# Optimization experiments

Measured on AMD Instinct MI355X. Metric: run time of the kernel, lower is better.

Reference implementation:

```python
import jax, jax.numpy as jnp
import numpy as np

B, S, D, H, F, E, K = 2, 2048, 1024, 16, 4096, 8, 2
EPS = 1e-6


def setup_inputs() -> dict:
    key = jax.random.key(0)
    ks = jax.random.split(key, 9)
    s = 0.02
    return {
        "x": jax.random.normal(ks[0], (B, S, D), jnp.float32),
        "n1_w": jnp.ones((D,), jnp.float32),
        "n2_w": jnp.ones((D,), jnp.float32),
        "wq": jax.random.normal(ks[1], (D, D), jnp.float32) * s,
        "wk": jax.random.normal(ks[2], (D, D), jnp.float32) * s,
        "wv": jax.random.normal(ks[3], (D, D), jnp.float32) * s,
        "wo": jax.random.normal(ks[4], (D, D), jnp.float32) * s,
        "router_w": jax.random.normal(ks[5], (E, D), jnp.float32) * s,  # nn.Linear(D, E, bias=False)
        "w1": jax.random.normal(ks[6], (E, D, F), jnp.float32) * s,
        "b1": jnp.zeros((E, F), jnp.float32),
        "w2": jax.random.normal(ks[7], (E, F, D), jnp.float32) * s,
        "b2": jnp.zeros((E, D), jnp.float32),
    }


def _rms(t, w):
    return t * w * jax.lax.rsqrt(jnp.mean(t * t, axis=-1, keepdims=True) + EPS)


def reference(x, n1_w, n2_w, wq, wk, wv, wo, router_w, w1, b1, w2, b2):
    hd = D // H
    # --- pre-norm causal multi-head self-attention ---
    h = _rms(x, n1_w)
    q = (h @ wq).reshape(B, S, H, hd)
    k = (h @ wk).reshape(B, S, H, hd)
    v = (h @ wv).reshape(B, S, H, hd)
    scores = jnp.einsum("bqhd,bkhd->bhqk", q, k) * (hd ** -0.5)
    causal = jnp.tril(jnp.ones((S, S), bool))
    scores = jnp.where(causal, scores, jnp.float32(-1e9))
    attn = jax.nn.softmax(scores, axis=-1)
    attn_out = jnp.einsum("bhqk,bkhd->bqhd", attn, v).reshape(B, S, D) @ wo
    x = x + attn_out
    # --- pre-norm MoE MLP: dense experts + top-k weighted combine ---
    h2 = _rms(x, n2_w)
    logits = h2 @ router_w.T                         # [B,S,E]
    probs = jax.nn.softmax(logits, axis=-1)
    topv, topi = jax.lax.top_k(probs, K)             # [B,S,K]
    topv = topv / jnp.sum(topv, axis=-1, keepdims=True)  # renormalized top-k gates
    bi = jnp.arange(B)[:, None, None]
    si = jnp.arange(S)[None, :, None]
    gates = jnp.zeros_like(probs).at[bi, si, topi].set(topv)  # sparse gates [B,S,E]
    eh = jax.nn.gelu(jnp.einsum("bsd,edf->ebsf", h2, w1) + b1[:, None, None, :])
    eo = jnp.einsum("ebsf,efd->ebsd", eh, w2) + b2[:, None, None, :]
    y = jnp.einsum("ebsd,bse->bsd", eo, gates)
    return x + y
```

## Files before the change

### kernel.cpp

```cpp
#include <hip/hip_runtime.h>
#include <hip/hip_bf16.h>


typedef float fx4 __attribute__((ext_vector_type(4)));
typedef short sx4 __attribute__((ext_vector_type(4)));
typedef short sx8 __attribute__((ext_vector_type(8)));
typedef int ix2 __attribute__((ext_vector_type(2)));
typedef int ix4 __attribute__((ext_vector_type(4)));

#define DEVFN static __device__ __forceinline__
#define MFMA16(a, b, c) __builtin_amdgcn_mfma_f32_16x16x32_bf16((a), (b), (c), 0, 0, 0)

typedef __attribute__((address_space(1))) const void GASV;
typedef __attribute__((address_space(3))) void LASV;

DEVFN short f2bf(float f) {
  unsigned u = __float_as_uint(f);
  return (short)((u + 0x7FFFu + ((u >> 16) & 1u)) >> 16);
}
DEVFN float bf2f(short s) { return __uint_as_float(((unsigned)(unsigned short)s) << 16); }

DEVFN int cvt_pk_bf16(float a, float b) {
  int r;
  asm("v_cvt_pk_bf16_f32 %0, %1, %2" : "=v"(r) : "v"(a), "v"(b));
  return r;
}

DEVFN void gll16(const short* g, short* l) {
  __builtin_amdgcn_global_load_lds((GASV*)g, (LASV*)l, 16, 0, 0);
}

DEVFN float fast_gelu(float x) {
  float u = 0.7978845608028654f * (x + 0.044715f * x * x * x);
  float e = __expf(2.0f * u);
  float t = 1.0f - 2.0f / (1.0f + e);
  return 0.5f * x * (1.0f + t);
}

DEVFN float wsum64(float v) {
#pragma unroll
  for (int m = 1; m < 64; m <<= 1) v += __shfl_xor(v, m);
  return v;
}

template <int SPLIT>
__global__ __launch_bounds__(256) void transpose_k(const float* in, short* oh, short* ol,
                                                   int R, int C) {
  __shared__ float t[64][65];
  const int c0 = blockIdx.x * 64, r0 = blockIdx.y * 64;
  const long long bofs = (long long)blockIdx.z * R * C;
  in += bofs;
  oh += bofs;
  if (SPLIT) ol += bofs;
  const int tid = threadIdx.x;
  const int rr = tid >> 4, cc4 = (tid & 15) * 4;
#pragma unroll
  for (int i = 0; i < 4; ++i) {
    int r = i * 16 + rr;
    fx4 v = *(const fx4*)(in + (long long)(r0 + r) * C + c0 + cc4);
    t[r][cc4] = v.x;
    t[r][cc4 + 1] = v.y;
    t[r][cc4 + 2] = v.z;
    t[r][cc4 + 3] = v.w;
  }
  __syncthreads();
#pragma unroll
  for (int i = 0; i < 4; ++i) {
    int oc = i * 16 + rr;
    sx4 hv, lv;
#pragma unroll
    for (int j = 0; j < 4; ++j) {
      float v = t[cc4 + j][oc];
      short hi = f2bf(v);
      hv[j] = hi;
      if (SPLIT) lv[j] = f2bf(v - bf2f(hi));
    }
    *(sx4*)(oh + (long long)(c0 + oc) * R + r0 + cc4) = hv;
    if (SPLIT) *(sx4*)(ol + (long long)(c0 + oc) * R + r0 + cc4) = lv;
  }
}

template <int SPLIT>
__global__ __launch_bounds__(256) void rms_k(const float* x, const float* w, short* hh,
                                             short* hl) {
  const int row = blockIdx.x, tid = threadIdx.x;
  const fx4 v = ((const fx4*)(x + (long long)row * 1024))[tid];
  float ss = v.x * v.x + v.y * v.y + v.z * v.z + v.w * v.w;
  ss = wsum64(ss);
  __shared__ float red[4];
  if ((tid & 63) == 0) red[tid >> 6] = ss;
  __syncthreads();
  ss = red[0] + red[1] + red[2] + red[3];
  const float rr = rsqrtf(ss * (1.0f / 1024.0f) + 1e-6f);
  const fx4 wv = ((const fx4*)w)[tid];
  float vals[4] = {v.x * wv.x * rr, v.y * wv.y * rr, v.z * wv.z * rr, v.w * wv.w * rr};
  sx4 oh, ol;
#pragma unroll
  for (int c = 0; c < 4; ++c) {
    short hi = f2bf(vals[c]);
    oh[c] = hi;
    if (SPLIT) ol[c] = f2bf(vals[c] - bf2f(hi));
  }
  ((sx4*)(hh + (long long)row * 1024))[tid] = oh;
  if (SPLIT) ((sx4*)(hl + (long long)row * 1024))[tid] = ol;
}

struct GemmArgs {
  const short *Ah, *Al, *Bh, *Bl;
  int K, lda, ldb, ldc;
  long long strideBe;
  short *out_h, *out_l;
  float* out_f;
  const float* bias;
  const int* tile_info;
  const float* row_gate;
};

template <int TERMS, int BK, int BN, int EPI, int PIPE>
__global__ __launch_bounds__(256) void gemm_k(GemmArgs a) {
  const int tid = threadIdx.x, lane = tid & 63, wave = tid >> 6;
  const int gx = gridDim.x;
  const int nwg = gx * (int)gridDim.y;
  int flat = (int)blockIdx.y * gx + (int)blockIdx.x;
  flat = (flat & 7) * (nwg >> 3) + (flat >> 3);
  const int bx = flat % gx;
  const int by = flat / gx;

  int row0, expert = 0, valid = 128;
  if constexpr (EPI == 3 || EPI == 5) {
    const int* ti = a.tile_info + by * 4;
    expert = ti[0];
    row0 = ti[1];
    valid = ti[2];
    if (valid == 0) return;
  } else {
    row0 = by * 128;
  }
  const short* Ap = a.Ah;
  const short* Bp = a.Bh + ((EPI == 3 || EPI == 5) ? (long long)expert * a.strideBe : 0ll);
  const int kbeg = blockIdx.z * a.K;

  constexpr int CH = BK / 8;
  constexpr int SW = (BK == 64) ? 7 : 3;
  constexpr int NIA = BK / 16;
  constexpr int NIB = (BN * CH) / 256;
  constexpr int ASZ = 128 * BK;
  constexpr int BSZ = BN * BK;
  constexpr int TN = BN / 32;
  constexpr int NB = PIPE ? 2 : 1;

  __shared__ short Ash[NB][ASZ];
  __shared__ short Bsh[NB][BSZ];
  __shared__ short Asl[TERMS == 3 ? NB : 1][TERMS == 3 ? ASZ : 1];
  __shared__ short Bsl[TERMS == 3 ? NB : 1][TERMS == 3 ? BSZ : 1];

  fx4 acc[4][TN] = {};
  const int wr = wave >> 1, wc = wave & 1;

  auto stage = [&](int s, int k0) {
#pragma unroll
    for (int i = 0; i < NIA; ++i) {
      int t = i * 256 + tid;
      int row = t / CH, c = t % CH;
      int cc = c ^ (row & SW);
      int lbase = (i * 256 + wave * 64) * 8;
      long long acol = kbeg + k0 + cc * 8;
      gll16(Ap + (long long)(row0 + row) * a.lda + acol, &Ash[s][lbase]);
      if constexpr (TERMS == 3)
        gll16(a.Al + (long long)(row0 + row) * a.lda + acol, &Asl[s][lbase]);
    }
#pragma unroll
    for (int i = 0; i < NIB; ++i) {
      int t = i * 256 + tid;
      int row = t / CH, c = t % CH;
      int cc = c ^ (row & SW);
      int lbase = (i * 256 + wave * 64) * 8;
      long long acol = kbeg + k0 + cc * 8;
      gll16(Bp + (long long)(bx * BN + row) * a.ldb + acol, &Bsh[s][lbase]);
      if constexpr (TERMS == 3)
        gll16(a.Bl + (long long)(bx * BN + row) * a.ldb + acol, &Bsl[s][lbase]);
    }
  };

  auto compute = [&](int s) {
#pragma unroll
    for (int kk = 0; kk < BK / 32; ++kk) {
      sx8 ah[4], bh[TN], al_[4], bl_[TN];
#pragma unroll
      for (int mi = 0; mi < 4; ++mi) {
        int row = wr * 64 + mi * 16 + (lane & 15);
        int sc = (kk * 4 + (lane >> 4)) ^ (row & SW);
        ah[mi] = *(const sx8*)&Ash[s][row * BK + sc * 8];
        if constexpr (TERMS == 3) al_[mi] = *(const sx8*)&Asl[s][row * BK + sc * 8];
      }
#pragma unroll
      for (int ni = 0; ni < TN; ++ni) {
        int row = wc * (BN / 2) + ni * 16 + (lane & 15);
        int sc = (kk * 4 + (lane >> 4)) ^ (row & SW);
        bh[ni] = *(const sx8*)&Bsh[s][row * BK + sc * 8];
        if constexpr (TERMS == 3) bl_[ni] = *(const sx8*)&Bsl[s][row * BK + sc * 8];
      }
#pragma unroll
      for (int mi = 0; mi < 4; ++mi)
#pragma unroll
        for (int ni = 0; ni < TN; ++ni) {
          acc[mi][ni] = MFMA16(ah[mi], bh[ni], acc[mi][ni]);
          if constexpr (TERMS == 3) {
            acc[mi][ni] = MFMA16(ah[mi], bl_[ni], acc[mi][ni]);
            acc[mi][ni] = MFMA16(al_[mi], bh[ni], acc[mi][ni]);
          }
        }
    }
  };

  const int NT = a.K / BK;
  stage(0, 0);
  __syncthreads();
  for (int t = 0; t < NT; ++t) {
    if constexpr (PIPE) {
      if (t + 1 < NT) stage((t + 1) & 1, (t + 1) * BK);
      compute(t & 1);
      if (t + 1 < NT) __syncthreads();
    } else {
      compute(0);
      if (t + 1 < NT) {
        __syncthreads();
        stage(0, (t + 1) * BK);
        __syncthreads();
      }
    }
  }

#pragma unroll
  for (int mi = 0; mi < 4; ++mi)
#pragma unroll
    for (int ni = 0; ni < TN; ++ni) {
      fx4 v = acc[mi][ni];
      int rl = wr * 64 + mi * 16 + ((lane >> 4) << 2);
      int col = bx * BN + wc * (BN / 2) + ni * 16 + (lane & 15);
#pragma unroll
      for (int j = 0; j < 4; ++j) {
        int r = rl + j;
        long long grow = (long long)row0 + r;
        float xv = v[j];
        if constexpr (EPI == 1) {
          short hi = f2bf(xv);
          a.out_h[grow * a.ldc + col] = hi;
          a.out_l[grow * a.ldc + col] = f2bf(xv - bf2f(hi));
        } else if constexpr (EPI == 3) {
          xv += a.bias[expert * a.ldc + col];
          a.out_h[grow * a.ldc + col] = f2bf(fast_gelu(xv));
        } else if constexpr (EPI == 5) {
          if (r < valid) {
            xv += a.bias[expert * a.ldc + col];
            float g = a.row_gate[grow];
            a.out_h[grow * a.ldc + col] = f2bf(xv * g);
          }
        } else if constexpr (EPI == 6) {
          a.out_f[(long long)blockIdx.z * 4194304 + grow * a.ldc + col] = xv;
        }
      }
    }
}

__global__ __launch_bounds__(256) void combine_wo_k(const float* p0, const float* p1,
                                                    const float* resid, float* out) {
  const long long i = ((long long)blockIdx.x * 256 + threadIdx.x) * 4;
  fx4 a = *(const fx4*)(p0 + i);
  fx4 b = *(const fx4*)(p1 + i);
  fx4 r = *(const fx4*)(resid + i);
  fx4 o;
#pragma unroll
  for (int j = 0; j < 4; ++j) o[j] = a[j] + b[j] + r[j];
  *(fx4*)(out + i) = o;
}

__global__ __launch_bounds__(256) void combine_k(const int* row_of_entry,
                                                 const short* eo, float* out) {
  const int tid = threadIdx.x, lane = tid & 63, wave = tid >> 6;
  const long long token = (long long)blockIdx.x * 4 + wave;
  const int r1 = row_of_entry[token * 2];
  const int r2 = row_of_entry[token * 2 + 1];
  const sx8* e1 = (const sx8*)(eo + (long long)r1 * 1024);
  const sx8* e2 = (const sx8*)(eo + (long long)r2 * 1024);
  float* op = out + token * 1024;
#pragma unroll
  for (int half = 0; half < 2; ++half) {
    sx8 va = e1[lane + half * 64];
    sx8 vb = e2[lane + half * 64];
    int cb = (lane + half * 64) * 8;
#pragma unroll
    for (int q = 0; q < 2; ++q) {
      fx4 o = *(const fx4*)(op + cb + q * 4);
#pragma unroll
      for (int j = 0; j < 4; ++j) o[j] += bf2f(va[q * 4 + j]) + bf2f(vb[q * 4 + j]);
      *(fx4*)(op + cb + q * 4) = o;
    }
  }
}

__global__ __launch_bounds__(128, 2) void flash_k(const short* __restrict__ qkv_h,
                                                  const short* __restrict__ qkv_l,
                                                  short* __restrict__ ao_h,
                                                  short* __restrict__ ao_l) {
  const int tid = threadIdx.x, lane = tid & 63, wave = tid >> 6;
  const int l15 = lane & 15, g = lane >> 4;
  const int qt = (blockIdx.x + blockIdx.y) & 31;
  const int bh = blockIdx.y;
  const int b = bh >> 4, h = bh & 15;
  const long long base = (long long)b * 2048 * 3072;
  const int qw = qt * 64 + wave * 32;

  __shared__ short Kh[4096], Kl[4096];
  __shared__ int VTh[64 * 34], VTl[64 * 34];

  sx8 qh[2][2], ql[2][2];
#pragma unroll
  for (int mb = 0; mb < 2; ++mb)
#pragma unroll
    for (int kk = 0; kk < 2; ++kk) {
      long long qofs =
          base + (long long)(qw + mb * 16 + l15) * 3072 + h * 64 + kk * 32 + g * 8;
      qh[mb][kk] = *(const sx8*)(qkv_h + qofs);
      ql[mb][kk] = *(const sx8*)(qkv_l + qofs);
    }

  fx4 o[2][4] = {};
  float m_r[2] = {-3e38f, -3e38f}, l_r[2] = {0.f, 0.f};

  const int krow0 = tid >> 3;
  const int kc8 = (tid & 7) * 8;
  const int kswz = ((tid & 7) ^ (krow0 & 7)) * 8;
  const int vu = tid >> 3;
  const int vd0 = (tid & 7) * 8;

  sx8 kr[4], krl[4], vr[4], vrl[4];

  auto load_tile = [&](int kt2) {
    const long long tb = base + (long long)(kt2 * 64) * 3072 + h * 64;
#pragma unroll
    for (int s = 0; s < 4; ++s) {
      long long gofs = tb + 1024 + (long long)(s * 16 + krow0) * 3072 + kc8;
      kr[s] = *(const sx8*)(qkv_h + gofs);
      krl[s] = *(const sx8*)(qkv_l + gofs);
    }
#pragma unroll
    for (int k4 = 0; k4 < 4; ++k4) {
      long long gofs = tb + 2048 + (long long)(4 * vu + k4) * 3072 + vd0;
      vr[k4] = *(const sx8*)(qkv_h + gofs);
      vrl[k4] = *(const sx8*)(qkv_l + gofs);
    }
  };

  const int nt = qt + 1;
  load_tile(0);

  for (int kt = 0; kt < nt; ++kt) {
#pragma unroll
    for (int s = 0; s < 4; ++s) {
      *(sx8*)&Kh[(s * 16 + krow0) * 64 + kswz] = kr[s];
      *(sx8*)&Kl[(s * 16 + krow0) * 64 + kswz] = krl[s];
    }
#pragma unroll
    for (int i = 0; i < 8; ++i) {
      int d = vd0 + i;
      ix2 wh, wl;
      wh[0] = (int)(unsigned short)vr[0][i] | ((int)(unsigned short)vr[1][i] << 16);
      wh[1] = (int)(unsigned short)vr[2][i] | ((int)(unsigned short)vr[3][i] << 16);
      wl[0] = (int)(unsigned short)vrl[0][i] | ((int)(unsigned short)vrl[1][i] << 16);
      wl[1] = (int)(unsigned short)vrl[2][i] | ((int)(unsigned short)vrl[3][i] << 16);
      *(ix2*)&VTh[d * 34 + 2 * vu] = wh;
      *(ix2*)&VTl[d * 34 + 2 * vu] = wl;
    }
    __syncthreads();

    if (kt + 1 < nt) load_tile(kt + 1);

    const bool diag = (kt == nt - 1);
    float pvv[2][16];
#pragma unroll
    for (int kc = 0; kc < 4; ++kc) {
      int row = kc * 16 + l15;
      int rsw = row & 7;
      fx4 s0 = {}, s1 = {};
#pragma unroll
      for (int kk = 0; kk < 2; ++kk) {
        int sc = ((kk * 4 + g) ^ rsw) * 8;
        sx8 khf = *(const sx8*)&Kh[row * 64 + sc];
        sx8 klf = *(const sx8*)&Kl[row * 64 + sc];
        s0 = MFMA16(khf, qh[0][kk], s0);
        s1 = MFMA16(khf, qh[1][kk], s1);
        s0 = MFMA16(khf, ql[0][kk], s0);
        s1 = MFMA16(khf, ql[1][kk], s1);
        s0 = MFMA16(klf, qh[0][kk], s0);
        s1 = MFMA16(klf, qh[1][kk], s1);
      }
#pragma unroll
      for (int j = 0; j < 4; ++j) {
        pvv[0][kc * 4 + j] = s0[j];
        pvv[1][kc * 4 + j] = s1[j];
      }
    }

    sx8 pah[2][2], pal[2][2];
#pragma unroll
    for (int mb = 0; mb < 2; ++mb) {
      const int qidx = qw + mb * 16 + l15;
      float t[16];
      float tmax = -3e38f;
#pragma unroll
      for (int i = 0; i < 16; ++i) {
        float sv = pvv[mb][i] * 0.18033688011112f;
        if (diag) {
          int key = kt * 64 + (i >> 2) * 16 + g * 4 + (i & 3);
          sv = (key > qidx) ? -3e38f : sv;
        }
        t[i] = sv;
        tmax = fmaxf(tmax, sv);
      }
      tmax = fmaxf(tmax, __shfl_xor(tmax, 16));
      tmax = fmaxf(tmax, __shfl_xor(tmax, 32));
      if (__any(tmax > m_r[mb] + 8.0f)) {
        float mnew = fmaxf(m_r[mb], tmax);
        float al = exp2f(m_r[mb] - mnew);
        l_r[mb] *= al;
        float aj[4];
#pragma unroll
        for (int j = 0; j < 4; ++j) aj[j] = __shfl(al, (lane & 48) | (g << 2) | j);
#pragma unroll
        for (int f = 0; f < 4; ++f)
#pragma unroll
          for (int j = 0; j < 4; ++j) o[mb][f][j] *= aj[j];
        m_r[mb] = mnew;
      }
      float ps = 0.f;
#pragma unroll
      for (int i = 0; i < 16; ++i) {
        float e = exp2f(t[i] - m_r[mb]);
        t[i] = e;
        ps += e;
      }
      l_r[mb] += ps;
#pragma unroll
      for (int grp = 0; grp < 2; ++grp) {
        ix4 ih, il;
#pragma unroll
        for (int q2 = 0; q2 < 4; ++q2) {
          float a = t[grp * 8 + 2 * q2], bb = t[grp * 8 + 2 * q2 + 1];
          int I = cvt_pk_bf16(a, bb);
          float h0 = __uint_as_float((unsigned)I << 16);
          float h1 = __uint_as_float((unsigned)I & 0xffff0000u);
          int L = cvt_pk_bf16(a - h0, bb - h1);
          ih[q2] = I;
          il[q2] = L;
        }
        pah[mb][grp] = __builtin_bit_cast(sx8, ih);
        pal[mb][grp] = __builtin_bit_cast(sx8, il);
      }
    }

    const ix2* vth = (const ix2*)VTh;
    const ix2* vtl = (const ix2*)VTl;
#pragma unroll
    for (int f = 0; f < 4; ++f) {
      int dd = f * 16 + l15;
      ix2 a0 = vth[dd * 17 + g], a1 = vth[dd * 17 + 4 + g];
      ix2 a2 = vth[dd * 17 + 8 + g], a3 = vth[dd * 17 + 12 + g];
      ix2 c0 = vtl[dd * 17 + g], c1 = vtl[dd * 17 + 4 + g];
      ix2 c2 = vtl[dd * 17 + 8 + g], c3 = vtl[dd * 17 + 12 + g];
      ix4 w;
      w[0] = a0[0]; w[1] = a0[1]; w[2] = a1[0]; w[3] = a1[1];
      sx8 vh8a = __builtin_bit_cast(sx8, w);
      w[0] = a2[0]; w[1] = a2[1]; w[2] = a3[0]; w[3] = a3[1];
      sx8 vh8b = __builtin_bit_cast(sx8, w);
      w[0] = c0[0]; w[1] = c0[1]; w[2] = c1[0]; w[3] = c1[1];
      sx8 vl8a = __builtin_bit_cast(sx8, w);
      w[0] = c2[0]; w[1] = c2[1]; w[2] = c3[0]; w[3] = c3[1];
      sx8 vl8b = __builtin_bit_cast(sx8, w);
#pragma unroll
      for (int mb = 0; mb < 2; ++mb) {
        o[mb][f] = MFMA16(pah[mb][0], vh8a, o[mb][f]);
        o[mb][f] = MFMA16(pah[mb][0], vl8a, o[mb][f]);
        o[mb][f] = MFMA16(pal[mb][0], vh8a, o[mb][f]);
        o[mb][f] = MFMA16(pah[mb][1], vh8b, o[mb][f]);
        o[mb][f] = MFMA16(pah[mb][1], vl8b, o[mb][f]);
        o[mb][f] = MFMA16(pal[mb][1], vh8b, o[mb][f]);
      }
    }
    __syncthreads();
  }

#pragma unroll
  for (int mb = 0; mb < 2; ++mb) {
    float lt = l_r[mb];
    lt += __shfl_xor(lt, 16);
    lt += __shfl_xor(lt, 32);
    float linv = 1.0f / lt;
    float lj[4];
#pragma unroll
    for (int j = 0; j < 4; ++j) lj[j] = __shfl(linv, (lane & 48) | (g << 2) | j);
#pragma unroll
    for (int f = 0; f < 4; ++f)
#pragma unroll
      for (int j = 0; j < 4; ++j) {
        float val = o[mb][f][j] * lj[j];
        long long orow = (long long)b * 2048 + qw + mb * 16 + g * 4 + j;
        int ocol = h * 64 + f * 16 + l15;
        short hi = f2bf(val);
        ao_h[orow * 1024 + ocol] = hi;
        ao_l[orow * 1024 + ocol] = f2bf(val - bf2f(hi));
      }
  }
}

__global__ __launch_bounds__(256) void router_k(const float* x2, const float* w,
                                                const float* rw, int* tok_e,
                                                float* tok_g) {
  const int tid = threadIdx.x, lane = tid & 63, wave = tid >> 6;
  const long long token = (long long)blockIdx.x * 4 + wave;
  const fx4* xr = (const fx4*)(x2 + token * 1024);
  const fx4* wr4 = (const fx4*)w;
  fx4 t[4];
  float ss = 0.0f;
#pragma unroll
  for (int i = 0; i < 4; ++i) {
    fx4 xv = xr[i * 64 + lane];
    fx4 wv = wr4[i * 64 + lane];
    ss += xv.x * xv.x + xv.y * xv.y + xv.z * xv.z + xv.w * xv.w;
    t[i].x = xv.x * wv.x;
    t[i].y = xv.y * wv.y;
    t[i].z = xv.z * wv.z;
    t[i].w = xv.w * wv.w;
  }
  ss = wsum64(ss);
  const float rr = rsqrtf(ss * (1.0f / 1024.0f) + 1e-6f);
  float logit[8];
#pragma unroll
  for (int e = 0; e < 8; ++e) {
    const fx4* re = (const fx4*)(rw + e * 1024);
    float acc = 0.0f;
#pragma unroll
    for (int i = 0; i < 4; ++i) {
      fx4 rv = re[i * 64 + lane];
      acc += t[i].x * rv.x + t[i].y * rv.y + t[i].z * rv.z + t[i].w * rv.w;
    }
    logit[e] = wsum64(acc) * rr;
  }
  float mx = logit[0];
#pragma unroll
  for (int e = 1; e < 8; ++e) mx = fmaxf(mx, logit[e]);
  float pe[8];
#pragma unroll
  for (int e = 0; e < 8; ++e) pe[e] = expf(logit[e] - mx);
  int e1 = 0;
  float b1v = pe[0];
#pragma unroll
  for (int e = 1; e < 8; ++e)
    if (pe[e] > b1v) {
      b1v = pe[e];
      e1 = e;
    }
  int e2 = -1;
  float b2v = -1.0f;
#pragma unroll
  for (int e = 0; e < 8; ++e)
    if (e != e1 && pe[e] > b2v) {
      b2v = pe[e];
      e2 = e;
    }
  if (lane == 0) {
    float inv = 1.0f / (b1v + b2v);
    tok_e[token * 2] = e1;
    tok_e[token * 2 + 1] = e2;
    tok_g[token * 2] = b1v * inv;
    tok_g[token * 2 + 1] = b2v * inv;
  }
}

__global__ __launch_bounds__(1024) void rank_k(const int* tok_e, const float* tok_g,
                                               int* tinfo, int* row_of_entry,
                                               int* row_token, float* row_gate) {
  const int tid = threadIdx.x, lane = tid & 63, wave = tid >> 6;
  __shared__ unsigned wtot[16][4];
  __shared__ unsigned woff[16][4];
  __shared__ int segsh[8];
  int e[8];
  {
    const int4* te = (const int4*)tok_e;
    int4 a = te[tid * 2], b = te[tid * 2 + 1];
    e[0] = a.x; e[1] = a.y; e[2] = a.z; e[3] = a.w;
    e[4] = b.x; e[5] = b.y; e[6] = b.z; e[7] = b.w;
  }
  unsigned c0 = 0, c1 = 0, c2 = 0, c3 = 0;
#pragma unroll
  for (int i = 0; i < 8; ++i) {
    unsigned f = 1u << ((e[i] & 1) << 4);
    int h = e[i] >> 1;
    c0 += (h == 0) ? f : 0u;
    c1 += (h == 1) ? f : 0u;
    c2 += (h == 2) ? f : 0u;
    c3 += (h == 3) ? f : 0u;
  }
  unsigned s0 = c0, s1 = c1, s2 = c2, s3 = c3;
#pragma unroll
  for (int d = 1; d < 64; d <<= 1) {
    unsigned t0 = __shfl_up(s0, d), t1 = __shfl_up(s1, d);
    unsigned t2 = __shfl_up(s2, d), t3 = __shfl_up(s3, d);
    if (lane >= d) { s0 += t0; s1 += t1; s2 += t2; s3 += t3; }
  }
  if (lane == 63) {
    wtot[wave][0] = s0; wtot[wave][1] = s1; wtot[wave][2] = s2; wtot[wave][3] = s3;
  }
  __syncthreads();
  if (wave == 0 && lane < 16) {
    unsigned v0 = wtot[lane][0], v1 = wtot[lane][1];
    unsigned v2 = wtot[lane][2], v3 = wtot[lane][3];
    unsigned i0 = v0, i1 = v1, i2 = v2, i3 = v3;
#pragma unroll
    for (int d = 1; d < 16; d <<= 1) {
      unsigned t0 = __shfl_up(i0, d), t1 = __shfl_up(i1, d);
      unsigned t2 = __shfl_up(i2, d), t3 = __shfl_up(i3, d);
      if (lane >= d) { i0 += t0; i1 += t1; i2 += t2; i3 += t3; }
    }
    woff[lane][0] = i0 - v0; woff[lane][1] = i1 - v1;
    woff[lane][2] = i2 - v2; woff[lane][3] = i3 - v3;
    if (lane == 15) {
      wtot[0][0] = i0; wtot[0][1] = i1; wtot[0][2] = i2; wtot[0][3] = i3;
    }
  }
  __syncthreads();
  if (tid == 0) {
    int cnt[8], tte[8], total = 0;
    for (int ee = 0; ee < 8; ++ee) {
      unsigned tot = wtot[0][ee >> 1];
      cnt[ee] = (int)((tot >> ((ee & 1) * 16)) & 0xFFFFu);
      tte[ee] = (cnt[ee] + 127) >> 7;
      total += tte[ee];
    }
    for (int s2 = 0; s2 < 80; ++s2) tinfo[s2 * 4 + 2] = 0;
    int off = 0, i = 0;
    for (int ee = 0; ee < 8; ++ee) {
      segsh[ee] = off;
      for (int t2 = 0; t2 < tte[ee]; ++t2) {
        int slot = (i * 80) / total;
        tinfo[slot * 4 + 0] = ee;
        tinfo[slot * 4 + 1] = off + t2 * 128;
        int v = cnt[ee] - t2 * 128;
        tinfo[slot * 4 + 2] = v > 128 ? 128 : v;
        ++i;
      }
      off += tte[ee] << 7;
    }
  }
  __syncthreads();
  unsigned x0 = woff[wave][0] + s0 - c0;
  unsigned x1 = woff[wave][1] + s1 - c1;
  unsigned x2 = woff[wave][2] + s2 - c2;
  unsigned x3 = woff[wave][3] + s3 - c3;
  const int entry0 = tid * 8;
#pragma unroll
  for (int i = 0; i < 8; ++i) {
    int ee = e[i];
    int h = ee >> 1, sh = (ee & 1) << 4;
    unsigned px = (h == 0) ? x0 : (h == 1) ? x1 : (h == 2) ? x2 : x3;
    int rank = (int)((px >> sh) & 0xFFFFu);
    unsigned f = 1u << sh;
    x0 += (h == 0) ? f : 0u;
    x1 += (h == 1) ? f : 0u;
    x2 += (h == 2) ? f : 0u;
    x3 += (h == 3) ? f : 0u;
    int row = segsh[ee] + rank;
    row_of_entry[entry0 + i] = row;
    row_token[row] = (entry0 + i) >> 1;
    row_gate[row] = tok_g[entry0 + i];
  }
}

__global__ __launch_bounds__(256) void gather_copy_k(const int* row_of_entry,
                                                     const short* h2, short* h2g) {
  const int tid = threadIdx.x, lane = tid & 63, wave = tid >> 6;
  const int entry = blockIdx.x * 4 + wave;
  const int token = entry >> 1;
  const int r = row_of_entry[entry];
  const sx8* src = (const sx8*)(h2 + (long long)token * 1024);
  sx8* dst = (sx8*)(h2g + (long long)r * 1024);
  dst[lane] = src[lane];
  dst[lane + 64] = src[lane + 64];
}

extern "C" void kernel_launch(void* const* d_in, const int* in_sizes, int n_in,
                              void* d_out, int out_size, void* d_ws, size_t ws_size,
                              hipStream_t stream) {
  (void)in_sizes;
  (void)n_in;
  (void)out_size;
  (void)ws_size;
  const float* x = (const float*)d_in[0];
  const float* n1w = (const float*)d_in[1];
  const float* n2w = (const float*)d_in[2];
  const float* wq = (const float*)d_in[3];
  const float* wk = (const float*)d_in[4];
  const float* wv = (const float*)d_in[5];
  const float* wo = (const float*)d_in[6];
  const float* rw = (const float*)d_in[7];
  const float* w1 = (const float*)d_in[8];
  const float* b1 = (const float*)d_in[9];
  const float* w2 = (const float*)d_in[10];
  const float* b2 = (const float*)d_in[11];
  float* out = (float*)d_out;
  char* ws = (char*)d_ws;

  short* wqkv_h = (short*)(ws + 0);
  short* wqkv_l = (short*)(ws + 6291456);
  short* wo_h = (short*)(ws + 12582912);
  short* wo_l = (short*)(ws + 14680064);
  short* h_h = (short*)(ws + 16777216);
  short* h_l = (short*)(ws + 25165824);
  short* qkv_h = (short*)(ws + 33554432);
  short* qkv_l = (short*)(ws + 58720256);
  short* ao_h = (short*)(ws + 83886080);
  short* ao_l = (short*)(ws + 92274688);
  float* wo_part = (float*)(ws + 100663296);
  short* h2 = (short*)(ws + 0);
  short* h2g = (short*)(ws + 8388608);
  short* eo = (short*)(ws + 8388608);
  short* wslot = (short*)(ws + 27262976);
  int* row_of_entry = (int*)(ws + 94371840);
  short* eh = (short*)(ws + 100663296);
  char* ctrl = ws + 176160768;
  int* tinfo = (int*)(ctrl + 128);
  int* tok_e = (int*)(ctrl + 2048);
  float* tok_g = (float*)(ctrl + 2048 + 32768);
  int* row_token = (int*)(ctrl + 2048 + 65536);
  float* row_gate = (float*)(ctrl + 2048 + 65536 + 36864);

  transpose_k<1><<<dim3(16, 16, 1), 256, 0, stream>>>(wq, wqkv_h, wqkv_l, 1024, 1024);
  transpose_k<1><<<dim3(16, 16, 1), 256, 0, stream>>>(wk, wqkv_h + 1024 * 1024,
                                                      wqkv_l + 1024 * 1024, 1024, 1024);
  transpose_k<1><<<dim3(16, 16, 1), 256, 0, stream>>>(wv, wqkv_h + 2048 * 1024,
                                                      wqkv_l + 2048 * 1024, 1024, 1024);
  transpose_k<1><<<dim3(16, 16, 1), 256, 0, stream>>>(wo, wo_h, wo_l, 1024, 1024);

  rms_k<1><<<4096, 256, 0, stream>>>(x, n1w, h_h, h_l);

  {
    GemmArgs a = {};
    a.Ah = h_h;
    a.Al = h_l;
    a.Bh = wqkv_h;
    a.Bl = wqkv_l;
    a.K = 1024;
    a.lda = 1024;
    a.ldb = 1024;
    a.ldc = 3072;
    a.out_h = qkv_h;
    a.out_l = qkv_l;
    gemm_k<3, 32, 128, 1, 1><<<dim3(24, 32), 256, 0, stream>>>(a);
  }

  flash_k<<<dim3(32, 32), 128, 0, stream>>>(qkv_h, qkv_l, ao_h, ao_l);

  {
    GemmArgs a = {};
    a.Ah = ao_h;
    a.Al = ao_l;
    a.Bh = wo_h;
    a.Bl = wo_l;
    a.K = 512;
    a.lda = 1024;
    a.ldb = 1024;
    a.ldc = 1024;
    a.out_f = wo_part;
    gemm_k<3, 32, 128, 6, 1><<<dim3(8, 32, 2), 256, 0, stream>>>(a);
  }
  combine_wo_k<<<4096, 256, 0, stream>>>(wo_part, wo_part + 4194304, x, out);

  rms_k<0><<<4096, 256, 0, stream>>>(out, n2w, h2, nullptr);
  router_k<<<1024, 256, 0, stream>>>(out, n2w, rw, tok_e, tok_g);
  rank_k<<<1, 1024, 0, stream>>>(tok_e, tok_g, tinfo, row_of_entry, row_token,
                                 row_gate);
  gather_copy_k<<<2048, 256, 0, stream>>>(row_of_entry, h2, h2g);

  transpose_k<0><<<dim3(64, 16, 8), 256, 0, stream>>>(w1, wslot, nullptr, 1024, 4096);
  {
    GemmArgs a = {};
    a.Ah = h2g;
    a.Bh = wslot;
    a.K = 1024;
    a.lda = 1024;
    a.ldb = 1024;
    a.ldc = 4096;
    a.strideBe = (long long)4096 * 1024;
    a.out_h = eh;
    a.bias = b1;
    a.tile_info = tinfo;
    gemm_k<1, 64, 128, 3, 0><<<dim3(32, 80), 256, 0, stream>>>(a);
  }

  transpose_k<0><<<dim3(16, 64, 8), 256, 0, stream>>>(w2, wslot, nullptr, 4096, 1024);
  {
    GemmArgs a = {};
    a.Ah = eh;
    a.Bh = wslot;
    a.K = 4096;
    a.lda = 4096;
    a.ldb = 4096;
    a.ldc = 1024;
    a.strideBe = (long long)1024 * 4096;
    a.out_h = eo;
    a.bias = b2;
    a.tile_info = tinfo;
    a.row_gate = row_gate;
    gemm_k<1, 64, 64, 5, 0><<<dim3(16, 80), 256, 0, stream>>>(a);
  }

  combine_k<<<1024, 256, 0, stream>>>(row_of_entry, eo, out);
}
```

Measured before the change: 683.1 us.

## Add triple-buffered GEMM pipeline with vmcnt waits and narrower tiles

Adds a PIPE==2 mode to the GEMM kernel that keeps three LDS stages and prefetches two K-tiles ahead. It waits on outstanding global-to-LDS loads with explicit s_waitcnt vmcnt counts instead of full syncthreads. The QKV and W1 GEMMs switch to this mode with BN halved to 64, doubling grid width, and the W2 GEMM moves from no pipelining to triple buffering. This aims to hide load latency and improve occupancy and balance. In exchange it uses more LDS and relies on exact load counts per stage being correct.

```diff
diff --git a/kernel.cpp b/kernel.cpp
--- a/kernel.cpp
+++ b/kernel.cpp
@@ -28,6 +28,17 @@
 
 DEVFN void gll16(const short* g, short* l) {
   __builtin_amdgcn_global_load_lds((GASV*)g, (LASV*)l, 16, 0, 0);
+}
+
+DEVFN void cfence() { asm volatile("" ::: "memory"); }
+
+template <int N>
+DEVFN void waitvm() {
+  if constexpr (N == 0) asm volatile("s_waitcnt vmcnt(0)" ::: "memory");
+  else if constexpr (N == 6) asm volatile("s_waitcnt vmcnt(6)" ::: "memory");
+  else if constexpr (N == 8) asm volatile("s_waitcnt vmcnt(8)" ::: "memory");
+  else if constexpr (N == 12) asm volatile("s_waitcnt vmcnt(12)" ::: "memory");
+  else if constexpr (N == 16) asm volatile("s_waitcnt vmcnt(16)" ::: "memory");
 }
 
 DEVFN float fast_gelu(float x) {
@@ -147,7 +158,8 @@
   constexpr int ASZ = 128 * BK;
   constexpr int BSZ = BN * BK;
   constexpr int TN = BN / 32;
-  constexpr int NB = PIPE ? 2 : 1;
+  constexpr int NB = (PIPE == 2) ? 3 : (PIPE == 1 ? 2 : 1);
+  constexpr int LPS = (NIA + NIB) * (TERMS == 3 ? 2 : 1);
 
   __shared__ short Ash[NB][ASZ];
   __shared__ short Bsh[NB][BSZ];
@@ -214,14 +226,33 @@
   };
 
   const int NT = a.K / BK;
-  stage(0, 0);
-  __syncthreads();
-  for (int t = 0; t < NT; ++t) {
-    if constexpr (PIPE) {
+  if constexpr (PIPE == 2) {
+    stage(0, 0);
+    if (NT > 1) stage(1, BK);
+    for (int t = 0; t < NT; ++t) {
+      __builtin_amdgcn_s_barrier();
+      cfence();
+      if (t + 2 < NT) stage((t + 2) % 3, (t + 2) * BK);
+      const int infl = (t + 1 < NT ? 1 : 0) + (t + 2 < NT ? 1 : 0);
+      if (infl == 2) waitvm<2 * LPS>();
+      else if (infl == 1) waitvm<LPS>();
+      else waitvm<0>();
+      __builtin_amdgcn_s_barrier();
+      cfence();
+      compute(t % 3);
+    }
+  } else if constexpr (PIPE == 1) {
+    stage(0, 0);
+    __syncthreads();
+    for (int t = 0; t < NT; ++t) {
       if (t + 1 < NT) stage((t + 1) & 1, (t + 1) * BK);
       compute(t & 1);
       if (t + 1 < NT) __syncthreads();
-    } else {
+    }
+  } else {
+    stage(0, 0);
+    __syncthreads();
+    for (int t = 0; t < NT; ++t) {
       compute(0);
       if (t + 1 < NT) {
         __syncthreads();
@@ -755,7 +786,7 @@
     a.ldc = 3072;
     a.out_h = qkv_h;
     a.out_l = qkv_l;
-    gemm_k<3, 32, 128, 1, 1><<<dim3(24, 32), 256, 0, stream>>>(a);
+    gemm_k<3, 32, 64, 1, 2><<<dim3(48, 32), 256, 0, stream>>>(a);
   }
 
   flash_k<<<dim3(32, 32), 128, 0, stream>>>(qkv_h, qkv_l, ao_h, ao_l);
@@ -794,7 +825,7 @@
     a.out_h = eh;
     a.bias = b1;
     a.tile_info = tinfo;
-    gemm_k<1, 64, 128, 3, 0><<<dim3(32, 80), 256, 0, stream>>>(a);
+    gemm_k<1, 64, 64, 3, 2><<<dim3(64, 80), 256, 0, stream>>>(a);
   }
 
   transpose_k<0><<<dim3(16, 64, 8), 256, 0, stream>>>(w2, wslot, nullptr, 4096, 1024);
@@ -811,7 +842,7 @@
     a.bias = b2;
     a.tile_info = tinfo;
     a.row_gate = row_gate;
-    gemm_k<1, 64, 64, 5, 0><<<dim3(16, 80), 256, 0, stream>>>(a);
+    gemm_k<1, 64, 64, 5, 2><<<dim3(16, 80), 256, 0, stream>>>(a);
   }
 
   combine_k<<<1024, 256, 0, stream>>>(row_of_entry, eo, out);
```

Result: slower. 789.7 us (+15.6%).

## Fuse token gather into expert GEMM A-loads and enable double-buffered pipelining

Applied to the files above, without the earlier changes.

Removes the separate gather_copy kernel by having the first expert GEMM load A rows indirectly through a per-row token index, precomputed once per thread. rank_k now zero-initialises row_token and row_gate so padded rows point at token 0 with zero gate. Both expert GEMMs switch from BK=64 single-buffered to BK=32 with double-buffered staging. This saves a full copy of the routed activations, at the cost of less contiguous A loads and a different pipeline/tile balance.

```diff
diff --git a/kernel.cpp b/kernel.cpp
--- a/kernel.cpp
+++ b/kernel.cpp
@@ -114,6 +114,7 @@
   const float* bias;
   const int* tile_info;
   const float* row_gate;
+  const int* row_token;
 };
 
 template <int TERMS, int BK, int BN, int EPI, int PIPE>
@@ -157,6 +158,16 @@
   fx4 acc[4][TN] = {};
   const int wr = wave >> 1, wc = wave & 1;
 
+  long long aoff[NIA];
+#pragma unroll
+  for (int i = 0; i < NIA; ++i) {
+    int row = (i * 256 + tid) / CH;
+    if constexpr (EPI == 3)
+      aoff[i] = (long long)a.row_token[row0 + row] * a.lda;
+    else
+      aoff[i] = (long long)(row0 + row) * a.lda;
+  }
+
   auto stage = [&](int s, int k0) {
 #pragma unroll
     for (int i = 0; i < NIA; ++i) {
@@ -165,9 +176,9 @@
       int cc = c ^ (row & SW);
       int lbase = (i * 256 + wave * 64) * 8;
       long long acol = kbeg + k0 + cc * 8;
-      gll16(Ap + (long long)(row0 + row) * a.lda + acol, &Ash[s][lbase]);
+      gll16(Ap + aoff[i] + acol, &Ash[s][lbase]);
       if constexpr (TERMS == 3)
-        gll16(a.Al + (long long)(row0 + row) * a.lda + acol, &Asl[s][lbase]);
+        gll16(a.Al + aoff[i] + acol, &Asl[s][lbase]);
     }
 #pragma unroll
     for (int i = 0; i < NIB; ++i) {
@@ -584,6 +595,14 @@
   __shared__ unsigned wtot[16][4];
   __shared__ unsigned woff[16][4];
   __shared__ int segsh[8];
+#pragma unroll
+  for (int i = 0; i < 9; ++i) {
+    int r = tid * 9 + i;
+    if (r < 9216) {
+      row_token[r] = 0;
+      row_gate[r] = 0.f;
+    }
+  }
   int e[8];
   {
     const int4* te = (const int4*)tok_e;
@@ -674,18 +693,6 @@
     row_token[row] = (entry0 + i) >> 1;
     row_gate[row] = tok_g[entry0 + i];
   }
-}
-
-__global__ __launch_bounds__(256) void gather_copy_k(const int* row_of_entry,
-                                                     const short* h2, short* h2g) {
-  const int tid = threadIdx.x, lane = tid & 63, wave = tid >> 6;
-  const int entry = blockIdx.x * 4 + wave;
-  const int token = entry >> 1;
-  const int r = row_of_entry[entry];
-  const sx8* src = (const sx8*)(h2 + (long long)token * 1024);
-  sx8* dst = (sx8*)(h2g + (long long)r * 1024);
-  dst[lane] = src[lane];
-  dst[lane + 64] = src[lane + 64];
 }
 
 extern "C" void kernel_launch(void* const* d_in, const int* in_sizes, int n_in,
@@ -722,7 +729,6 @@
   short* ao_l = (short*)(ws + 92274688);
   float* wo_part = (float*)(ws + 100663296);
   short* h2 = (short*)(ws + 0);
-  short* h2g = (short*)(ws + 8388608);
   short* eo = (short*)(ws + 8388608);
   short* wslot = (short*)(ws + 27262976);
   int* row_of_entry = (int*)(ws + 94371840);
@@ -779,12 +785,11 @@
   router_k<<<1024, 256, 0, stream>>>(out, n2w, rw, tok_e, tok_g);
   rank_k<<<1, 1024, 0, stream>>>(tok_e, tok_g, tinfo, row_of_entry, row_token,
                                  row_gate);
-  gather_copy_k<<<2048, 256, 0, stream>>>(row_of_entry, h2, h2g);
 
   transpose_k<0><<<dim3(64, 16, 8), 256, 0, stream>>>(w1, wslot, nullptr, 1024, 4096);
   {
     GemmArgs a = {};
-    a.Ah = h2g;
+    a.Ah = h2;
     a.Bh = wslot;
     a.K = 1024;
     a.lda = 1024;
@@ -794,7 +799,8 @@
     a.out_h = eh;
     a.bias = b1;
     a.tile_info = tinfo;
-    gemm_k<1, 64, 128, 3, 0><<<dim3(32, 80), 256, 0, stream>>>(a);
+    a.row_token = row_token;
+    gemm_k<1, 32, 128, 3, 1><<<dim3(32, 80), 256, 0, stream>>>(a);
   }
 
   transpose_k<0><<<dim3(16, 64, 8), 256, 0, stream>>>(w2, wslot, nullptr, 4096, 1024);
@@ -811,7 +817,7 @@
     a.bias = b2;
     a.tile_info = tinfo;
     a.row_gate = row_gate;
-    gemm_k<1, 64, 64, 5, 0><<<dim3(16, 80), 256, 0, stream>>>(a);
+    gemm_k<1, 32, 64, 5, 1><<<dim3(16, 80), 256, 0, stream>>>(a);
   }
 
   combine_k<<<1024, 256, 0, stream>>>(row_of_entry, eo, out);
```

After: 639.9 us. 1.07x faster.
